# Kernel optimization log

Hardware: AMD Instinct MI355X
Metric: run time of the kernel (lower is better)

Reference implementation:

```python
import jax, jax.numpy as jnp
import numpy as np

K = 20  # n_knn

def knn_idx(x, k):
    # x: (B, C, N) -> (B, N, k) indices of k nearest neighbors (by neg sq dist)
    xx = jnp.sum(x * x, axis=1)                      # (B, N)
    inner = jnp.einsum('bcn,bcm->bnm', x, x)          # (B, N, N)
    neg_dist = 2.0 * inner - xx[:, :, None] - xx[:, None, :]
    _, idx = jax.lax.top_k(neg_dist, k)               # (B, N, k)
    return idx

def get_graph_feature(x, k):
    # x: (B, C, N) -> (B, 2C, N, k) with channels [x_j - x_i, x_i]
    idx = knn_idx(x, k)                               # (B, N, k)
    feats = jnp.transpose(x, (0, 2, 1))               # (B, N, C)
    neighbors = jax.vmap(lambda f, i: f[i])(feats, idx)   # (B, N, k, C)
    center = feats[:, :, None, :]                     # (B, N, 1, C)
    center_b = jnp.broadcast_to(center, neighbors.shape)
    feat = jnp.concatenate([neighbors - center_b, center_b], axis=-1)  # (B,N,k,2C)
    return jnp.transpose(feat, (0, 3, 1, 2))          # (B, 2C, N, k)

def edge_conv(x, w, s, b, k):
    # 1x1 conv (no bias) + folded eval-BN affine + LeakyReLU(0.2), then max over k
    g = get_graph_feature(x, k)                       # (B, 2C, N, k)
    y = jnp.einsum('bcnk,oc->bonk', g, w)
    y = y * s[None, :, None, None] + b[None, :, None, None]
    y = jnp.where(y >= 0, y, 0.2 * y)
    return jnp.max(y, axis=-1)                        # (B, O, N)

def setup_inputs() -> dict:
    key = jax.random.key(0)
    ks = jax.random.split(key, 16)
    d = {'x': jax.random.normal(ks[0], (16, 3, 1024), dtype=jnp.float32)}
    dims = [(64, 6), (64, 128), (128, 128), (256, 256), (512, 512)]
    for i, (o, c) in enumerate(dims):
        d[f'w{i+1}'] = jax.random.normal(ks[3*i+1], (o, c), dtype=jnp.float32) * (1.0 / np.sqrt(c))
        d[f's{i+1}'] = jax.random.uniform(ks[3*i+2], (o,), dtype=jnp.float32, minval=0.5, maxval=1.5)
        d[f'b{i+1}'] = jax.random.normal(ks[3*i+3], (o,), dtype=jnp.float32) * 0.1
    return d

def reference(x, w1, s1, b1, w2, s2, b2, w3, s3, b3, w4, s4, b4, w5, s5, b5):
    x1 = edge_conv(x, w1, s1, b1, K)    # (B, 64, N)
    x2 = edge_conv(x1, w2, s2, b2, K)   # (B, 64, N)
    x3 = edge_conv(x2, w3, s3, b3, K)   # (B, 128, N)
    x4 = edge_conv(x3, w4, s4, b4, K)   # (B, 256, N)
    xc = jnp.concatenate([x1, x2, x3, x4], axis=1)  # (B, 512, N)
    y = jnp.einsum('bcn,oc->bon', xc, w5)
    y = y * s5[None, :, None] + b5[None, :, None]
    x_inv = jnp.where(y >= 0, y, 0.2 * y)            # (B, feat_dim, N)
    p_max = jnp.max(x_inv, axis=-1)                  # (B, feat_dim)
    p_avg = jnp.mean(x_inv, axis=-1)                 # (B, feat_dim)
    x_equ = jnp.concatenate([p_max, p_avg], axis=1)  # (B, 2*feat_dim)
    return (x_equ, x_inv)
```

## Files before the change

kernel.cpp:

```cpp
#include <hip/hip_runtime.h>
#include <hip/hip_bf16.h>

#define NPTS 1024
#define KNN_K 20

template<int C>
__global__ __launch_bounds__(256)
void knn_kernel(const float* __restrict__ x, int* __restrict__ knn_idx,
                int in_bstride)
{
    __shared__ float dist[8][NPTS];
    __shared__ float xn[8][C < 4 ? 4 : C];
    __shared__ float xxr[8];
    const int b  = blockIdx.x >> 7;
    const int n0 = (blockIdx.x & 127) << 3;
    const int tid = threadIdx.x;
    const float* xb = x + (size_t)b * in_bstride;

    for (int i = tid; i < 8 * C; i += 256) {
        const int r = i / C, c = i - r * C;
        xn[r][c] = xb[c * NPTS + n0 + r];
    }
    __syncthreads();
    if (tid < 8) {
        float s = 0.f;
        for (int c = 0; c < C; c++) s = fmaf(xn[tid][c], xn[tid][c], s);
        xxr[tid] = s;
    }
    __syncthreads();

    float acc[8][4];
    #pragma unroll
    for (int r = 0; r < 8; r++)
        acc[r][0] = acc[r][1] = acc[r][2] = acc[r][3] = 0.f;
    float sq[4] = {0.f, 0.f, 0.f, 0.f};
    const int m0 = tid * 4;

    if constexpr (C % 4 == 0) {
        for (int c4 = 0; c4 < C; c4 += 4) {
            float4 xnv[8];
            #pragma unroll
            for (int r = 0; r < 8; r++)
                xnv[r] = *reinterpret_cast<const float4*>(&xn[r][c4]);
            #pragma unroll
            for (int u = 0; u < 4; u++) {
                const float4 xm = *reinterpret_cast<const float4*>(xb + (c4 + u) * NPTS + m0);
                sq[0] = fmaf(xm.x, xm.x, sq[0]);
                sq[1] = fmaf(xm.y, xm.y, sq[1]);
                sq[2] = fmaf(xm.z, xm.z, sq[2]);
                sq[3] = fmaf(xm.w, xm.w, sq[3]);
                #pragma unroll
                for (int r = 0; r < 8; r++) {
                    const float xv = (u == 0) ? xnv[r].x : (u == 1) ? xnv[r].y
                                   : (u == 2) ? xnv[r].z : xnv[r].w;
                    acc[r][0] = fmaf(xv, xm.x, acc[r][0]);
                    acc[r][1] = fmaf(xv, xm.y, acc[r][1]);
                    acc[r][2] = fmaf(xv, xm.z, acc[r][2]);
                    acc[r][3] = fmaf(xv, xm.w, acc[r][3]);
                }
            }
        }
    } else {
        for (int c = 0; c < C; c++) {
            const float4 xm = *reinterpret_cast<const float4*>(xb + c * NPTS + m0);
            sq[0] = fmaf(xm.x, xm.x, sq[0]);
            sq[1] = fmaf(xm.y, xm.y, sq[1]);
            sq[2] = fmaf(xm.z, xm.z, sq[2]);
            sq[3] = fmaf(xm.w, xm.w, sq[3]);
            #pragma unroll
            for (int r = 0; r < 8; r++) {
                const float xv = xn[r][c];
                acc[r][0] = fmaf(xv, xm.x, acc[r][0]);
                acc[r][1] = fmaf(xv, xm.y, acc[r][1]);
                acc[r][2] = fmaf(xv, xm.z, acc[r][2]);
                acc[r][3] = fmaf(xv, xm.w, acc[r][3]);
            }
        }
    }
    #pragma unroll
    for (int r = 0; r < 8; r++) {
        float4 dv;
        dv.x = 2.f * acc[r][0] - xxr[r] - sq[0];
        dv.y = 2.f * acc[r][1] - xxr[r] - sq[1];
        dv.z = 2.f * acc[r][2] - xxr[r] - sq[2];
        dv.w = 2.f * acc[r][3] - xxr[r] - sq[3];
        *reinterpret_cast<float4*>(&dist[r][m0]) = dv;
    }
    __syncthreads();

    const int r    = tid >> 5;
    const int lane = tid & 31;
    float v[32];
    #pragma unroll
    for (int q = 0; q < 32; q++) v[q] = dist[r][lane + 32 * q];

    float lv = v[0]; int lq = 0;
    #pragma unroll
    for (int q = 1; q < 32; q++) if (v[q] > lv) { lv = v[q]; lq = q; }

    int* outp = knn_idx + ((size_t)(b * NPTS + n0 + r)) * KNN_K;
    for (int k = 0; k < KNN_K; k++) {
        float bv_ = lv;
        int   bm  = lane + 32 * lq;
        #pragma unroll
        for (int off = 16; off; off >>= 1) {
            const float ov = __shfl_xor(bv_, off, 32);
            const int   om = __shfl_xor(bm, off, 32);
            if (ov > bv_ || (ov == bv_ && om < bm)) { bv_ = ov; bm = om; }
        }
        if (lane == 0) outp[k] = bm;
        const int wl = bm & 31, wq = bm >> 5;
        if (lane == wl) {
            #pragma unroll
            for (int q = 0; q < 32; q++) if (q == wq) v[q] = -INFINITY;
            lv = v[0]; lq = 0;
            #pragma unroll
            for (int q = 1; q < 32; q++) if (v[q] > lv) { lv = v[q]; lq = q; }
        }
    }
}

template<bool DUAL>
__global__ __launch_bounds__(256)
void mm_kernel(const float* __restrict__ xin, const float* __restrict__ w,
               float* __restrict__ Z, float* __restrict__ Z2,
               int C, int O, int in_bstride, int wstride)
{
    __shared__ float xs[32][64];
    __shared__ float ws1[32][68];
    __shared__ float ws2[32][68];
    const int n0 = blockIdx.x * 64;
    const int o0 = blockIdx.y * 64;
    const int b  = blockIdx.z;
    const int tid = threadIdx.x;
    const int nl = (tid & 15) * 4;
    const int ol = (tid >> 4) * 4;
    float a1[4][4] = {{0.f}};
    float a2[4][4] = {{0.f}};
    const float* xb = xin + (size_t)b * in_bstride;

    for (int cc = 0; cc < C; cc += 32) {
        #pragma unroll
        for (int t = 0; t < 8; t++) {
            const int id = tid + t * 256;
            const int j = id >> 6, nn = id & 63;
            const int c = cc + j;
            xs[j][nn] = (c < C) ? xb[c * NPTS + n0 + nn] : 0.f;
        }
        #pragma unroll
        for (int t = 0; t < 8; t++) {
            const int id = tid + t * 256;
            const int j = id & 31, i = id >> 5;
            const int c = cc + j;
            ws1[j][i] = (c < C) ? w[(o0 + i) * wstride + c] : 0.f;
            if (DUAL) ws2[j][i] = (c < C) ? w[(o0 + i) * wstride + C + c] : 0.f;
        }
        __syncthreads();
        #pragma unroll
        for (int j = 0; j < 32; j++) {
            const float4 xv = *reinterpret_cast<const float4*>(&xs[j][nl]);
            const float4 wv = *reinterpret_cast<const float4*>(&ws1[j][ol]);
            const float xr[4] = {xv.x, xv.y, xv.z, xv.w};
            const float wr[4] = {wv.x, wv.y, wv.z, wv.w};
            #pragma unroll
            for (int oi = 0; oi < 4; oi++)
                #pragma unroll
                for (int ni = 0; ni < 4; ni++)
                    a1[oi][ni] = fmaf(wr[oi], xr[ni], a1[oi][ni]);
            if (DUAL) {
                const float4 w2 = *reinterpret_cast<const float4*>(&ws2[j][ol]);
                const float w2r[4] = {w2.x, w2.y, w2.z, w2.w};
                #pragma unroll
                for (int oi = 0; oi < 4; oi++)
                    #pragma unroll
                    for (int ni = 0; ni < 4; ni++)
                        a2[oi][ni] = fmaf(w2r[oi], xr[ni], a2[oi][ni]);
            }
        }
        __syncthreads();
    }

    #pragma unroll
    for (int oi = 0; oi < 4; oi++) {
        const int o = o0 + ol + oi;
        const float4 r1 = make_float4(a1[oi][0], a1[oi][1], a1[oi][2], a1[oi][3]);
        *reinterpret_cast<float4*>(Z + ((size_t)b * O + o) * NPTS + n0 + nl) = r1;
        if (DUAL) {
            const float4 r2 = make_float4(a2[oi][0], a2[oi][1], a2[oi][2], a2[oi][3]);
            *reinterpret_cast<float4*>(Z2 + ((size_t)b * O + o) * NPTS + n0 + nl) = r2;
        }
    }
}

__global__ __launch_bounds__(256)
void mm5_kernel(const float* __restrict__ xin, const float* __restrict__ w,
                const float* __restrict__ sv, const float* __restrict__ bvec,
                float* __restrict__ out)
{
    __shared__ float xs[32][128];
    __shared__ float ws[32][128];
    const int n0 = blockIdx.x * 128;
    const int o0 = blockIdx.y * 128;
    const int b  = blockIdx.z;
    const int tid = threadIdx.x;
    const int nl = (tid & 15) * 8;
    const int ol = (tid >> 4) * 8;
    float acc[8][8] = {{0.f}};
    const float* xb = xin + (size_t)b * (512 * NPTS);

    for (int cc = 0; cc < 512; cc += 32) {
        #pragma unroll
        for (int t = 0; t < 4; t++) {
            const int f = tid + t * 256;
            const int j = f >> 5, col = (f & 31) * 4;
            *reinterpret_cast<float4*>(&xs[j][col]) =
                *reinterpret_cast<const float4*>(&xb[(cc + j) * NPTS + n0 + col]);
        }
        #pragma unroll
        for (int t = 0; t < 4; t++) {
            const int id = tid + t * 256;
            const int i = id & 127, jq = (id >> 7) * 4;
            const float4 wv = *reinterpret_cast<const float4*>(&w[(o0 + i) * 512 + cc + jq]);
            ws[jq + 0][i] = wv.x;
            ws[jq + 1][i] = wv.y;
            ws[jq + 2][i] = wv.z;
            ws[jq + 3][i] = wv.w;
        }
        __syncthreads();
        #pragma unroll
        for (int j = 0; j < 32; j++) {
            float xr[8], wr[8];
            *reinterpret_cast<float4*>(&xr[0]) = *reinterpret_cast<const float4*>(&xs[j][nl]);
            *reinterpret_cast<float4*>(&xr[4]) = *reinterpret_cast<const float4*>(&xs[j][nl + 4]);
            *reinterpret_cast<float4*>(&wr[0]) = *reinterpret_cast<const float4*>(&ws[j][ol]);
            *reinterpret_cast<float4*>(&wr[4]) = *reinterpret_cast<const float4*>(&ws[j][ol + 4]);
            #pragma unroll
            for (int oi = 0; oi < 8; oi++)
                #pragma unroll
                for (int ni = 0; ni < 8; ni++)
                    acc[oi][ni] = fmaf(wr[oi], xr[ni], acc[oi][ni]);
        }
        __syncthreads();
    }

    #pragma unroll
    for (int oi = 0; oi < 8; oi++) {
        const int o = o0 + ol + oi;
        const float s = sv[o], bb = bvec[o];
        float* zp = out + ((size_t)b * 512 + o) * NPTS + n0 + nl;
        #pragma unroll
        for (int h = 0; h < 2; h++) {
            float4 r;
            r.x = fmaf(s, acc[oi][h * 4 + 0], bb);
            r.y = fmaf(s, acc[oi][h * 4 + 1], bb);
            r.z = fmaf(s, acc[oi][h * 4 + 2], bb);
            r.w = fmaf(s, acc[oi][h * 4 + 3], bb);
            r.x = r.x >= 0.f ? r.x : 0.2f * r.x;
            r.y = r.y >= 0.f ? r.y : 0.2f * r.y;
            r.z = r.z >= 0.f ? r.z : 0.2f * r.z;
            r.w = r.w >= 0.f ? r.w : 0.2f * r.w;
            *reinterpret_cast<float4*>(zp + h * 4) = r;
        }
    }
}

__global__ __launch_bounds__(256)
void gather_kernel(const float* __restrict__ Z, const float* __restrict__ Z2,
                   const int* __restrict__ knn_idx,
                   const float* __restrict__ sv, const float* __restrict__ bvec,
                   float* __restrict__ outc, int O, int ch_off)
{
    __shared__ int idx_s[64][21];
    const int n0  = blockIdx.x * 64;
    const int og0 = blockIdx.y * 16;
    const int b   = blockIdx.z;
    const int tid = threadIdx.x;
    const int* ig = knn_idx + (size_t)(b * NPTS + n0) * KNN_K;
    for (int i = tid; i < 64 * KNN_K; i += 256) {
        const int nn = i / KNN_K, k = i - nn * KNN_K;
        idx_s[nn][k] = ig[i];
    }
    __syncthreads();
    const int nn = tid & 63;
    const int oo = tid >> 6;
    const int n  = n0 + nn;
    for (int oc = 0; oc < 16; oc += 4) {
        const int o = og0 + oc + oo;
        const float* zr = Z + ((size_t)b * O + o) * NPTS;
        float mx = -INFINITY;
        #pragma unroll
        for (int k = 0; k < KNN_K; k++)
            mx = fmaxf(mx, zr[idx_s[nn][k]]);
        const float cz = zr[n];
        const float z2 = Z2[((size_t)b * O + o) * NPTS + n];
        float y = fmaf(sv[o], (mx - cz + z2), bvec[o]);
        y = y >= 0.f ? y : 0.2f * y;
        outc[(size_t)b * (512 * NPTS) + (size_t)(ch_off + o) * NPTS + n] = y;
    }
}

__global__ __launch_bounds__(256)
void reduce_kernel(const float* __restrict__ xinv, float* __restrict__ xequ)
{
    const int b = blockIdx.x >> 9;
    const int o = blockIdx.x & 511;
    const float* row = xinv + (size_t)blockIdx.x * NPTS;
    const int tid = threadIdx.x;
    const float4 val = *reinterpret_cast<const float4*>(&row[tid * 4]);
    float mx = fmaxf(fmaxf(val.x, val.y), fmaxf(val.z, val.w));
    float sm = (val.x + val.y) + (val.z + val.w);
    #pragma unroll
    for (int off = 32; off; off >>= 1) {
        mx = fmaxf(mx, __shfl_down(mx, off));
        sm += __shfl_down(sm, off);
    }
    __shared__ float smx[4], ssm[4];
    if ((tid & 63) == 0) { smx[tid >> 6] = mx; ssm[tid >> 6] = sm; }
    __syncthreads();
    if (tid == 0) {
        mx = fmaxf(fmaxf(smx[0], smx[1]), fmaxf(smx[2], smx[3]));
        sm = (ssm[0] + ssm[1]) + (ssm[2] + ssm[3]);
        xequ[b * 1024 + o] = mx;
        xequ[b * 1024 + 512 + o] = sm * (1.0f / 1024.0f);
    }
}

extern "C" void kernel_launch(void* const* d_in, const int* in_sizes, int n_in,
                              void* d_out, int out_size, void* d_ws, size_t ws_size,
                              hipStream_t stream)
{
    const float* x  = (const float*)d_in[0];
    const float* w1 = (const float*)d_in[1],  *s1 = (const float*)d_in[2],  *b1 = (const float*)d_in[3];
    const float* w2 = (const float*)d_in[4],  *s2 = (const float*)d_in[5],  *b2 = (const float*)d_in[6];
    const float* w3 = (const float*)d_in[7],  *s3 = (const float*)d_in[8],  *b3 = (const float*)d_in[9];
    const float* w4 = (const float*)d_in[10], *s4 = (const float*)d_in[11], *b4 = (const float*)d_in[12];
    const float* w5 = (const float*)d_in[13], *s5 = (const float*)d_in[14], *b5 = (const float*)d_in[15];

    float* out  = (float*)d_out;
    float* xequ = out;
    float* xinv = out + 16 * 1024;

    float* xc  = (float*)d_ws;
    float* Z   = xc  + (size_t)16 * 512 * NPTS;
    float* Z2  = Z   + (size_t)16 * 256 * NPTS;
    int*   idxb = (int*)(Z2 + (size_t)16 * 256 * NPTS);

    const int BS_XC = 512 * NPTS;

    knn_kernel<3><<<2048, 256, 0, stream>>>(x, idxb, 3 * NPTS);
    mm_kernel<true><<<dim3(16, 1, 16), 256, 0, stream>>>(
        x, w1, Z, Z2, 3, 64, 3 * NPTS, 6);
    gather_kernel<<<dim3(16, 4, 16), 256, 0, stream>>>(Z, Z2, idxb, s1, b1, xc, 64, 0);

    knn_kernel<64><<<2048, 256, 0, stream>>>(xc, idxb, BS_XC);
    mm_kernel<true><<<dim3(16, 1, 16), 256, 0, stream>>>(
        xc, w2, Z, Z2, 64, 64, BS_XC, 128);
    gather_kernel<<<dim3(16, 4, 16), 256, 0, stream>>>(Z, Z2, idxb, s2, b2, xc, 64, 64);

    {
        const float* in3 = xc + (size_t)64 * NPTS;
        knn_kernel<64><<<2048, 256, 0, stream>>>(in3, idxb, BS_XC);
        mm_kernel<true><<<dim3(16, 2, 16), 256, 0, stream>>>(
            in3, w3, Z, Z2, 64, 128, BS_XC, 128);
        gather_kernel<<<dim3(16, 8, 16), 256, 0, stream>>>(Z, Z2, idxb, s3, b3, xc, 128, 128);
    }

    {
        const float* in4 = xc + (size_t)128 * NPTS;
        knn_kernel<128><<<2048, 256, 0, stream>>>(in4, idxb, BS_XC);
        mm_kernel<true><<<dim3(16, 4, 16), 256, 0, stream>>>(
            in4, w4, Z, Z2, 128, 256, BS_XC, 256);
        gather_kernel<<<dim3(16, 16, 16), 256, 0, stream>>>(Z, Z2, idxb, s4, b4, xc, 256, 256);
    }

    mm5_kernel<<<dim3(8, 4, 16), 256, 0, stream>>>(xc, w5, s5, b5, xinv);

    reduce_kernel<<<8192, 256, 0, stream>>>(xinv, xequ);
}
```

Baseline: 851.0 us.

## Halve knn rows per block using full-wave selection; stage Z rows in LDS for gather

The knn kernel now handles 4 query points per block instead of 8 and runs top-k selection across a full 64-lane wavefront with 16 values per lane. This doubles the grid size and cuts per-thread register arrays, which should raise occupancy and shorten the serial argmax rescans. The gather kernel now loads a 16-channel by 1024-point tile of Z into LDS (64 KB), so the neighbor max reads hit shared memory rather than random global addresses. The trade-off is lower gather occupancy from the large LDS allocation, and the knn kernel rereads the candidate point features from global memory twice as often.

```diff
diff --git a/kernel.cpp b/kernel.cpp
--- a/kernel.cpp
+++ b/kernel.cpp
@@ -9,38 +9,38 @@
 void knn_kernel(const float* __restrict__ x, int* __restrict__ knn_idx,
                 int in_bstride)
 {
-    __shared__ float dist[8][NPTS];
-    __shared__ float xn[8][C < 4 ? 4 : C];
-    __shared__ float xxr[8];
-    const int b  = blockIdx.x >> 7;
-    const int n0 = (blockIdx.x & 127) << 3;
+    __shared__ float dist[4][NPTS];
+    __shared__ float xn[4][C < 4 ? 4 : C];
+    __shared__ float xxr[4];
+    const int b  = blockIdx.x >> 8;
+    const int n0 = (blockIdx.x & 255) << 2;
     const int tid = threadIdx.x;
     const float* xb = x + (size_t)b * in_bstride;
 
-    for (int i = tid; i < 8 * C; i += 256) {
+    for (int i = tid; i < 4 * C; i += 256) {
         const int r = i / C, c = i - r * C;
         xn[r][c] = xb[c * NPTS + n0 + r];
     }
     __syncthreads();
-    if (tid < 8) {
+    if (tid < 4) {
         float s = 0.f;
         for (int c = 0; c < C; c++) s = fmaf(xn[tid][c], xn[tid][c], s);
         xxr[tid] = s;
     }
     __syncthreads();
 
-    float acc[8][4];
-    #pragma unroll
-    for (int r = 0; r < 8; r++)
+    float acc[4][4];
+    #pragma unroll
+    for (int r = 0; r < 4; r++)
         acc[r][0] = acc[r][1] = acc[r][2] = acc[r][3] = 0.f;
     float sq[4] = {0.f, 0.f, 0.f, 0.f};
     const int m0 = tid * 4;
 
     if constexpr (C % 4 == 0) {
         for (int c4 = 0; c4 < C; c4 += 4) {
-            float4 xnv[8];
-            #pragma unroll
-            for (int r = 0; r < 8; r++)
+            float4 xnv[4];
+            #pragma unroll
+            for (int r = 0; r < 4; r++)
                 xnv[r] = *reinterpret_cast<const float4*>(&xn[r][c4]);
             #pragma unroll
             for (int u = 0; u < 4; u++) {
@@ -50,7 +50,7 @@
                 sq[2] = fmaf(xm.z, xm.z, sq[2]);
                 sq[3] = fmaf(xm.w, xm.w, sq[3]);
                 #pragma unroll
-                for (int r = 0; r < 8; r++) {
+                for (int r = 0; r < 4; r++) {
                     const float xv = (u == 0) ? xnv[r].x : (u == 1) ? xnv[r].y
                                    : (u == 2) ? xnv[r].z : xnv[r].w;
                     acc[r][0] = fmaf(xv, xm.x, acc[r][0]);
@@ -68,7 +68,7 @@
             sq[2] = fmaf(xm.z, xm.z, sq[2]);
             sq[3] = fmaf(xm.w, xm.w, sq[3]);
             #pragma unroll
-            for (int r = 0; r < 8; r++) {
+            for (int r = 0; r < 4; r++) {
                 const float xv = xn[r][c];
                 acc[r][0] = fmaf(xv, xm.x, acc[r][0]);
                 acc[r][1] = fmaf(xv, xm.y, acc[r][1]);
@@ -78,7 +78,7 @@
         }
     }
     #pragma unroll
-    for (int r = 0; r < 8; r++) {
+    for (int r = 0; r < 4; r++) {
         float4 dv;
         dv.x = 2.f * acc[r][0] - xxr[r] - sq[0];
         dv.y = 2.f * acc[r][1] - xxr[r] - sq[1];
@@ -88,34 +88,34 @@
     }
     __syncthreads();
 
-    const int r    = tid >> 5;
-    const int lane = tid & 31;
-    float v[32];
-    #pragma unroll
-    for (int q = 0; q < 32; q++) v[q] = dist[r][lane + 32 * q];
+    const int r    = tid >> 6;
+    const int lane = tid & 63;
+    float v[16];
+    #pragma unroll
+    for (int q = 0; q < 16; q++) v[q] = dist[r][lane + 64 * q];
 
     float lv = v[0]; int lq = 0;
     #pragma unroll
-    for (int q = 1; q < 32; q++) if (v[q] > lv) { lv = v[q]; lq = q; }
+    for (int q = 1; q < 16; q++) if (v[q] > lv) { lv = v[q]; lq = q; }
 
     int* outp = knn_idx + ((size_t)(b * NPTS + n0 + r)) * KNN_K;
     for (int k = 0; k < KNN_K; k++) {
         float bv_ = lv;
-        int   bm  = lane + 32 * lq;
-        #pragma unroll
-        for (int off = 16; off; off >>= 1) {
-            const float ov = __shfl_xor(bv_, off, 32);
-            const int   om = __shfl_xor(bm, off, 32);
+        int   bm  = lane + 64 * lq;
+        #pragma unroll
+        for (int off = 32; off; off >>= 1) {
+            const float ov = __shfl_xor(bv_, off);
+            const int   om = __shfl_xor(bm, off);
             if (ov > bv_ || (ov == bv_ && om < bm)) { bv_ = ov; bm = om; }
         }
         if (lane == 0) outp[k] = bm;
-        const int wl = bm & 31, wq = bm >> 5;
+        const int wl = bm & 63, wq = bm >> 6;
         if (lane == wl) {
             #pragma unroll
-            for (int q = 0; q < 32; q++) if (q == wq) v[q] = -INFINITY;
+            for (int q = 0; q < 16; q++) if (q == wq) v[q] = -INFINITY;
             lv = v[0]; lq = 0;
             #pragma unroll
-            for (int q = 1; q < 32; q++) if (v[q] > lv) { lv = v[q]; lq = q; }
+            for (int q = 1; q < 16; q++) if (v[q] > lv) { lv = v[q]; lq = q; }
         }
     }
 }
@@ -268,34 +268,43 @@
 void gather_kernel(const float* __restrict__ Z, const float* __restrict__ Z2,
                    const int* __restrict__ knn_idx,
                    const float* __restrict__ sv, const float* __restrict__ bvec,
-                   float* __restrict__ outc, int O, int ch_off)
-{
-    __shared__ int idx_s[64][21];
-    const int n0  = blockIdx.x * 64;
-    const int og0 = blockIdx.y * 16;
+                   float* __restrict__ outc, int O, int ch_off, int nper)
+{
+    __shared__ float zs[16][NPTS];
+    const int ot  = blockIdx.x * 16;
+    const int n00 = blockIdx.y * nper;
     const int b   = blockIdx.z;
     const int tid = threadIdx.x;
-    const int* ig = knn_idx + (size_t)(b * NPTS + n0) * KNN_K;
-    for (int i = tid; i < 64 * KNN_K; i += 256) {
-        const int nn = i / KNN_K, k = i - nn * KNN_K;
-        idx_s[nn][k] = ig[i];
-    }
-    __syncthreads();
-    const int nn = tid & 63;
-    const int oo = tid >> 6;
-    const int n  = n0 + nn;
-    for (int oc = 0; oc < 16; oc += 4) {
-        const int o = og0 + oc + oo;
-        const float* zr = Z + ((size_t)b * O + o) * NPTS;
-        float mx = -INFINITY;
-        #pragma unroll
-        for (int k = 0; k < KNN_K; k++)
-            mx = fmaxf(mx, zr[idx_s[nn][k]]);
-        const float cz = zr[n];
-        const float z2 = Z2[((size_t)b * O + o) * NPTS + n];
-        float y = fmaf(sv[o], (mx - cz + z2), bvec[o]);
-        y = y >= 0.f ? y : 0.2f * y;
-        outc[(size_t)b * (512 * NPTS) + (size_t)(ch_off + o) * NPTS + n] = y;
+    const float* Zb = Z + ((size_t)b * O + ot) * NPTS;
+
+    #pragma unroll
+    for (int t = 0; t < 16; t++) {
+        const int f = tid + t * 256;
+        const int row = f >> 8, col = (f & 255) * 4;
+        *reinterpret_cast<float4*>(&zs[row][col]) =
+            *reinterpret_cast<const float4*>(&Zb[row * NPTS + col]);
+    }
+    __syncthreads();
+
+    for (int nc = 0; nc < nper; nc += 256) {
+        const int n = n00 + nc + tid;
+        const int* ip = knn_idx + ((size_t)(b * NPTS + n)) * KNN_K;
+        int idx[KNN_K];
+        #pragma unroll
+        for (int k = 0; k < KNN_K; k++) idx[k] = ip[k];
+        #pragma unroll 4
+        for (int oi = 0; oi < 16; oi++) {
+            float mx = -INFINITY;
+            #pragma unroll
+            for (int k = 0; k < KNN_K; k++)
+                mx = fmaxf(mx, zs[oi][idx[k]]);
+            const int o = ot + oi;
+            const float cz = zs[oi][n];
+            const float z2 = Z2[((size_t)b * O + o) * NPTS + n];
+            float y = fmaf(sv[o], (mx - cz + z2), bvec[o]);
+            y = y >= 0.f ? y : 0.2f * y;
+            outc[(size_t)b * (512 * NPTS) + (size_t)(ch_off + o) * NPTS + n] = y;
+        }
     }
 }
 
@@ -347,30 +356,30 @@
 
     const int BS_XC = 512 * NPTS;
 
-    knn_kernel<3><<<2048, 256, 0, stream>>>(x, idxb, 3 * NPTS);
+    knn_kernel<3><<<4096, 256, 0, stream>>>(x, idxb, 3 * NPTS);
     mm_kernel<true><<<dim3(16, 1, 16), 256, 0, stream>>>(
         x, w1, Z, Z2, 3, 64, 3 * NPTS, 6);
-    gather_kernel<<<dim3(16, 4, 16), 256, 0, stream>>>(Z, Z2, idxb, s1, b1, xc, 64, 0);
-
-    knn_kernel<64><<<2048, 256, 0, stream>>>(xc, idxb, BS_XC);
+    gather_kernel<<<dim3(4, 4, 16), 256, 0, stream>>>(Z, Z2, idxb, s1, b1, xc, 64, 0, 256);
+
+    knn_kernel<64><<<4096, 256, 0, stream>>>(xc, idxb, BS_XC);
     mm_kernel<true><<<dim3(16, 1, 16), 256, 0, stream>>>(
         xc, w2, Z, Z2, 64, 64, BS_XC, 128);
-    gather_kernel<<<dim3(16, 4, 16), 256, 0, stream>>>(Z, Z2, idxb, s2, b2, xc, 64, 64);
+    gather_kernel<<<dim3(4, 4, 16), 256, 0, stream>>>(Z, Z2, idxb, s2, b2, xc, 64, 64, 256);
 
     {
         const float* in3 = xc + (size_t)64 * NPTS;
-        knn_kernel<64><<<2048, 256, 0, stream>>>(in3, idxb, BS_XC);
+        knn_kernel<64><<<4096, 256, 0, stream>>>(in3, idxb, BS_XC);
         mm_kernel<true><<<dim3(16, 2, 16), 256, 0, stream>>>(
             in3, w3, Z, Z2, 64, 128, BS_XC, 128);
-        gather_kernel<<<dim3(16, 8, 16), 256, 0, stream>>>(Z, Z2, idxb, s3, b3, xc, 128, 128);
+        gather_kernel<<<dim3(8, 2, 16), 256, 0, stream>>>(Z, Z2, idxb, s3, b3, xc, 128, 128, 512);
     }
 
     {
         const float* in4 = xc + (size_t)128 * NPTS;
-        knn_kernel<128><<<2048, 256, 0, stream>>>(in4, idxb, BS_XC);
+        knn_kernel<128><<<4096, 256, 0, stream>>>(in4, idxb, BS_XC);
         mm_kernel<true><<<dim3(16, 4, 16), 256, 0, stream>>>(
             in4, w4, Z, Z2, 128, 256, BS_XC, 256);
-        gather_kernel<<<dim3(16, 16, 16), 256, 0, stream>>>(Z, Z2, idxb, s4, b4, xc, 256, 256);
+        gather_kernel<<<dim3(16, 1, 16), 256, 0, stream>>>(Z, Z2, idxb, s4, b4, xc, 256, 256, 1024);
     }
 
     mm5_kernel<<<dim3(8, 4, 16), 256, 0, stream>>>(xc, w5, s5, b5, xinv);
```

After: 755.3 us. 1.13x faster.
